# Performance work log

Hardware: AMD Instinct MI355X
Metric: run time of the kernel (lower is better)

The kernel has to match this reference:

```python
import jax, jax.numpy as jnp
import numpy as np

B, N = 16, 200000
R = 1_000_000
ITERS = 5
DAMPING = 0.5


def setup_inputs() -> dict:
    key = jax.random.key(0)
    ks = jax.random.split(key, 7)
    return {
        "evidence_logits": jax.random.normal(ks[0], (B, N), dtype=jnp.float32),
        "weights_t1": jax.random.uniform(ks[1], (R,), dtype=jnp.float32),
        "weights_t2": jax.random.uniform(ks[2], (R,), dtype=jnp.float32),
        "weights_t3": jax.random.uniform(ks[3], (R,), dtype=jnp.float32),
        "indices_t1": jax.random.randint(ks[4], (R, 2), 0, N, dtype=jnp.int64) if jax.config.jax_enable_x64 else jax.random.randint(ks[4], (R, 2), 0, N, dtype=jnp.int32),
        "indices_t2": jax.random.randint(ks[5], (R, 3), 0, N, dtype=jnp.int32),
        "indices_t3": jax.random.randint(ks[6], (R, 3), 0, N, dtype=jnp.int32),
    }


def _t1_messages(q, idx, w):
    # Template T1: p_a -> p_c
    a, c = idx[:, 0], idx[:, 1]
    q_a = q[:, a]            # (B, R)
    q_c = q[:, c]
    wb = w[None, :]
    delta = jnp.zeros_like(q)
    delta = delta.at[:, c].add(wb * q_a)
    delta = delta.at[:, a].add(wb * (q_c - 1.0))
    return delta


def _t2_messages(q, idx, w):
    # Template T2: p_a ^ p_b -> p_c
    a, b, c = idx[:, 0], idx[:, 1], idx[:, 2]
    q_a, q_b, q_c = q[:, a], q[:, b], q[:, c]
    wb = w[None, :]
    delta = jnp.zeros_like(q)
    delta = delta.at[:, c].add(wb * q_a * q_b)
    delta = delta.at[:, a].add(wb * q_b * (q_c - 1.0))
    delta = delta.at[:, b].add(wb * q_a * (q_c - 1.0))
    return delta


def _t3_messages(q, idx, w):
    # Template T3: p_a ^ !p_b -> p_c
    a, b, c = idx[:, 0], idx[:, 1], idx[:, 2]
    q_a, q_b, q_c = q[:, a], q[:, b], q[:, c]
    wb = w[None, :]
    delta = jnp.zeros_like(q)
    delta = delta.at[:, c].add(wb * q_a * (1.0 - q_b))
    delta = delta.at[:, a].add(wb * (1.0 - q_b) * (q_c - 1.0))
    delta = delta.at[:, b].add(wb * q_a * (1.0 - q_c))
    return delta


def reference(evidence_logits, weights_t1, weights_t2, weights_t3,
              indices_t1, indices_t2, indices_t3):
    curr_logits = evidence_logits
    curr_q = jax.nn.sigmoid(curr_logits)
    for _ in range(ITERS):
        total = (_t1_messages(curr_q, indices_t1, weights_t1)
                 + _t2_messages(curr_q, indices_t2, weights_t2)
                 + _t3_messages(curr_q, indices_t3, weights_t3))
        target_logits = evidence_logits + total
        curr_logits = (1.0 - DAMPING) * curr_logits + DAMPING * target_logits
        curr_q = jax.nn.sigmoid(curr_logits)
    return curr_q
```

## Files before the change

kernel.cpp:

```cpp
#include <hip/hip_runtime.h>

#define B 16
#define NN 200000
#define R 1000000
#define ITERS 5

__device__ __forceinline__ float sigmoidf_(float x) {
    return 1.0f / (1.0f + __expf(-x));
}

__global__ void cavi_init(const float* __restrict__ ev,
                          float* __restrict__ logits,
                          float* __restrict__ q_nb,
                          float* __restrict__ delta_nb) {
    int i = blockIdx.x * blockDim.x + threadIdx.x;
    if (i >= NN * B) return;
    int b = i & 15, n = i >> 4;
    float e = ev[b * NN + n];
    logits[b * NN + n] = e;
    q_nb[i] = sigmoidf_(e);
    delta_nb[i] = 0.0f;
}

__global__ void cavi_edges(const float* __restrict__ q,
                           float* __restrict__ delta,
                           const int* __restrict__ idx1, const float* __restrict__ w1,
                           const int* __restrict__ idx2, const float* __restrict__ w2,
                           const int* __restrict__ idx3, const float* __restrict__ w3) {
    int gid = blockIdx.x * blockDim.x + threadIdx.x;
    int b = gid & 15;
    int e = gid >> 4;
    if (e >= 3 * R) return;
    if (e < R) {
        int a = idx1[e * 2 + 0];
        int c = idx1[e * 2 + 1];
        float w = w1[e];
        float qa = q[a * B + b];
        float qc = q[c * B + b];
        atomicAdd(&delta[c * B + b], w * qa);
        atomicAdd(&delta[a * B + b], w * (qc - 1.0f));
    } else if (e < 2 * R) {
        int ei = e - R;
        int a  = idx2[ei * 3 + 0];
        int bb = idx2[ei * 3 + 1];
        int c  = idx2[ei * 3 + 2];
        float w = w2[ei];
        float qa = q[a * B + b];
        float qb = q[bb * B + b];
        float qc = q[c * B + b];
        atomicAdd(&delta[c * B + b],  w * qa * qb);
        atomicAdd(&delta[a * B + b],  w * qb * (qc - 1.0f));
        atomicAdd(&delta[bb * B + b], w * qa * (qc - 1.0f));
    } else {
        int ei = e - 2 * R;
        int a  = idx3[ei * 3 + 0];
        int bb = idx3[ei * 3 + 1];
        int c  = idx3[ei * 3 + 2];
        float w = w3[ei];
        float qa = q[a * B + b];
        float qb = q[bb * B + b];
        float qc = q[c * B + b];
        atomicAdd(&delta[c * B + b],  w * qa * (1.0f - qb));
        atomicAdd(&delta[a * B + b],  w * (1.0f - qb) * (qc - 1.0f));
        atomicAdd(&delta[bb * B + b], w * qa * (1.0f - qc));
    }
}

__global__ void cavi_update(const float* __restrict__ ev,
                            float* __restrict__ logits,
                            float* __restrict__ q_nb,
                            float* __restrict__ delta_nb,
                            int write_q) {
    int i = blockIdx.x * blockDim.x + threadIdx.x;
    if (i >= NN * B) return;
    int b = i & 15, n = i >> 4;
    float d = delta_nb[i];
    delta_nb[i] = 0.0f;
    float e  = ev[b * NN + n];
    float cl = logits[b * NN + n];
    float nl = 0.5f * cl + 0.5f * (e + d);
    float qv = sigmoidf_(nl);
    q_nb[i] = qv;
    logits[b * NN + n] = write_q ? qv : nl;
}

extern "C" void kernel_launch(void* const* d_in, const int* in_sizes, int n_in,
                              void* d_out, int out_size, void* d_ws, size_t ws_size,
                              hipStream_t stream) {
    const float* ev   = (const float*)d_in[0];
    const float* w1   = (const float*)d_in[1];
    const float* w2   = (const float*)d_in[2];
    const float* w3   = (const float*)d_in[3];
    const int*   idx1 = (const int*)d_in[4];
    const int*   idx2 = (const int*)d_in[5];
    const int*   idx3 = (const int*)d_in[6];

    float* logits   = (float*)d_out;
    float* q_nb     = (float*)d_ws;
    float* delta_nb = q_nb + (size_t)NN * B;

    const int ethreads = 256;
    const int nb_total = NN * B;
    const int nb_grid  = (nb_total + ethreads - 1) / ethreads;
    const int edge_total = 3 * R * B;
    const int edge_grid  = (edge_total + ethreads - 1) / ethreads;

    cavi_init<<<nb_grid, ethreads, 0, stream>>>(ev, logits, q_nb, delta_nb);
    for (int it = 0; it < ITERS; ++it) {
        cavi_edges<<<edge_grid, ethreads, 0, stream>>>(q_nb, delta_nb,
                                                       idx1, w1, idx2, w2, idx3, w3);
        cavi_update<<<nb_grid, ethreads, 0, stream>>>(ev, logits, q_nb, delta_nb,
                                                      it == ITERS - 1 ? 1 : 0);
    }
}
```

Baseline: 2.052 ms.

## Replace atomic scatter with CSR gather built per call for message passing

Builds a destination-indexed CSR (count, scan, fill) of all 8M edge contributions each call. Each iteration then becomes an atomic-free gather kernel that fuses the damping and sigmoid update, with q double-buffered. Evidence and output are transposed through LDS into node-major layout. This removes float atomics, but adds a per-call build pass with integer atomics and 96MB of extra workspace. It falls back to the old path if the workspace is too small.

```diff
diff --git a/kernel.cpp b/kernel.cpp
--- a/kernel.cpp
+++ b/kernel.cpp
@@ -4,15 +4,189 @@
 #define NN 200000
 #define R 1000000
 #define ITERS 5
+#define E_TOT (8 * R)
+#define SCAN_B 1024
+
+typedef unsigned int uint;
 
 __device__ __forceinline__ float sigmoidf_(float x) {
     return 1.0f / (1.0f + __expf(-x));
 }
 
-__global__ void cavi_init(const float* __restrict__ ev,
-                          float* __restrict__ logits,
-                          float* __restrict__ q_nb,
-                          float* __restrict__ delta_nb) {
+
+__global__ void cavi_zero_u32(uint* __restrict__ p, int n) {
+    int i = blockIdx.x * blockDim.x + threadIdx.x;
+    if (i < n) p[i] = 0u;
+}
+
+__global__ void cavi_count(const int* __restrict__ i1, const int* __restrict__ i2,
+                           const int* __restrict__ i3, uint* __restrict__ cnt) {
+    int e = blockIdx.x * blockDim.x + threadIdx.x;
+    if (e >= R) return;
+    int a1 = i1[2 * e], c1 = i1[2 * e + 1];
+    atomicAdd(&cnt[c1], 1u); atomicAdd(&cnt[a1], 1u);
+    int a2 = i2[3 * e], b2 = i2[3 * e + 1], c2 = i2[3 * e + 2];
+    atomicAdd(&cnt[c2], 1u); atomicAdd(&cnt[a2], 1u); atomicAdd(&cnt[b2], 1u);
+    int a3 = i3[3 * e], b3 = i3[3 * e + 1], c3 = i3[3 * e + 2];
+    atomicAdd(&cnt[c3], 1u); atomicAdd(&cnt[a3], 1u); atomicAdd(&cnt[b3], 1u);
+}
+
+__global__ void cavi_scan1(uint* __restrict__ cnt, uint* __restrict__ bsum) {
+    __shared__ uint s[SCAN_B];
+    int i = blockIdx.x * SCAN_B + threadIdx.x;
+    uint v = (i < NN) ? cnt[i] : 0u;
+    s[threadIdx.x] = v;
+    __syncthreads();
+    for (int d = 1; d < SCAN_B; d <<= 1) {
+        uint t = (threadIdx.x >= d) ? s[threadIdx.x - d] : 0u;
+        __syncthreads();
+        s[threadIdx.x] += t;
+        __syncthreads();
+    }
+    if (i < NN) cnt[i] = s[threadIdx.x] - v;
+    if (threadIdx.x == SCAN_B - 1) bsum[blockIdx.x] = s[threadIdx.x];
+}
+
+__global__ void cavi_scan2(uint* __restrict__ bsum, int nb) {
+    __shared__ uint s[256];
+    uint v = (threadIdx.x < (uint)nb) ? bsum[threadIdx.x] : 0u;
+    s[threadIdx.x] = v;
+    __syncthreads();
+    for (int d = 1; d < 256; d <<= 1) {
+        uint t = (threadIdx.x >= d) ? s[threadIdx.x - d] : 0u;
+        __syncthreads();
+        s[threadIdx.x] += t;
+        __syncthreads();
+    }
+    if (threadIdx.x < (uint)nb) bsum[threadIdx.x] = s[threadIdx.x] - v;
+    if (threadIdx.x == 255) bsum[nb] = s[255];
+}
+
+__global__ void cavi_scan3(const uint* __restrict__ cnt, const uint* __restrict__ bsum,
+                           uint* __restrict__ off, uint* __restrict__ cursor, int nb) {
+    int i = blockIdx.x * blockDim.x + threadIdx.x;
+    if (i < NN) {
+        uint v = cnt[i] + bsum[i >> 10];
+        off[i] = v;
+        cursor[i] = v;
+    } else if (i == NN) {
+        off[NN] = bsum[nb];
+    }
+}
+
+__device__ __forceinline__ void put_entry(int dest, int s1, uint md1, int s2, uint md2, float w,
+                                          uint* __restrict__ cursor, uint* __restrict__ m0,
+                                          uint* __restrict__ m1, float* __restrict__ wf) {
+    uint pos = atomicAdd(&cursor[dest], 1u);
+    m0[pos] = (uint)s1 | (md1 << 18);
+    m1[pos] = (uint)s2 | (md2 << 18);
+    wf[pos] = w;
+}
+
+__global__ void cavi_fill(const int* __restrict__ i1, const float* __restrict__ w1,
+                          const int* __restrict__ i2, const float* __restrict__ w2,
+                          const int* __restrict__ i3, const float* __restrict__ w3,
+                          uint* __restrict__ cursor, uint* __restrict__ m0,
+                          uint* __restrict__ m1, float* __restrict__ wf) {
+    int e = blockIdx.x * blockDim.x + threadIdx.x;
+    if (e >= R) return;
+    {
+        int a = i1[2 * e], c = i1[2 * e + 1];
+        float w = w1[e];
+        put_entry(c, a, 0u, 0, 3u, w, cursor, m0, m1, wf);
+        put_entry(a, c, 1u, 0, 3u, w, cursor, m0, m1, wf);
+    }
+    {
+        int a = i2[3 * e], b = i2[3 * e + 1], c = i2[3 * e + 2];
+        float w = w2[e];
+        put_entry(c, a, 0u, b, 0u, w, cursor, m0, m1, wf);
+        put_entry(a, b, 0u, c, 1u, w, cursor, m0, m1, wf);
+        put_entry(b, a, 0u, c, 1u, w, cursor, m0, m1, wf);
+    }
+    {
+        int a = i3[3 * e], b = i3[3 * e + 1], c = i3[3 * e + 2];
+        float w = w3[e];
+        put_entry(c, a, 0u, b, 2u, w, cursor, m0, m1, wf);
+        put_entry(a, b, 2u, c, 1u, w, cursor, m0, m1, wf);
+        put_entry(b, a, 0u, c, 2u, w, cursor, m0, m1, wf);
+    }
+}
+
+
+__global__ void cavi_init_tp(const float* __restrict__ ev, float* __restrict__ ev_nb,
+                             float* __restrict__ logits_nb, float* __restrict__ q0) {
+    __shared__ float lds[64 * 17];
+    int n0 = blockIdx.x * 64;
+    #pragma unroll
+    for (int p = 0; p < 4; ++p) {
+        int idx = p * 256 + threadIdx.x;
+        int b = idx >> 6, i = idx & 63;
+        lds[i * 17 + b] = ev[b * NN + n0 + i];
+    }
+    __syncthreads();
+    #pragma unroll
+    for (int p = 0; p < 4; ++p) {
+        int j = p * 256 + threadIdx.x;
+        int i = j >> 4, b = j & 15;
+        float v = lds[i * 17 + b];
+        int o = n0 * B + j;
+        ev_nb[o] = v;
+        logits_nb[o] = v;
+        q0[o] = sigmoidf_(v);
+    }
+}
+
+__global__ void cavi_out_tp(const float* __restrict__ q_nb, float* __restrict__ out) {
+    __shared__ float lds[64 * 17];
+    int n0 = blockIdx.x * 64;
+    #pragma unroll
+    for (int p = 0; p < 4; ++p) {
+        int j = p * 256 + threadIdx.x;
+        int i = j >> 4, b = j & 15;
+        lds[i * 17 + b] = q_nb[n0 * B + j];
+    }
+    __syncthreads();
+    #pragma unroll
+    for (int p = 0; p < 4; ++p) {
+        int idx = p * 256 + threadIdx.x;
+        int b = idx >> 6, i = idx & 63;
+        out[b * NN + n0 + i] = lds[i * 17 + b];
+    }
+}
+
+
+__global__ void cavi_main(const uint* __restrict__ off,
+                          const uint* __restrict__ m0, const uint* __restrict__ m1,
+                          const float* __restrict__ wf,
+                          const float* __restrict__ ev_nb, float* __restrict__ logits_nb,
+                          const float* __restrict__ q_in, float* __restrict__ q_out) {
+    int t = blockIdx.x * blockDim.x + threadIdx.x;
+    if (t >= NN * B) return;
+    int n = t >> 4, b = t & 15;
+    uint k0 = off[n], k1 = off[n + 1];
+    float acc = 0.0f;
+    for (uint k = k0; k < k1; ++k) {
+        uint a0 = m0[k], a1 = m1[k];
+        float w = wf[k];
+        float x = q_in[((a0 & 0x3FFFFu) << 4) + b];
+        uint md1 = a0 >> 18;
+        x = (md1 == 0u) ? x : ((md1 == 1u) ? x - 1.0f : 1.0f - x);
+        uint md2 = a1 >> 18;
+        float y = 1.0f;
+        if (md2 != 3u) {
+            float q2 = q_in[((a1 & 0x3FFFFu) << 4) + b];
+            y = (md2 == 0u) ? q2 : ((md2 == 1u) ? q2 - 1.0f : 1.0f - q2);
+        }
+        acc = fmaf(w * x, y, acc);
+    }
+    float nl = 0.5f * logits_nb[t] + 0.5f * (ev_nb[t] + acc);
+    logits_nb[t] = nl;
+    q_out[t] = sigmoidf_(nl);
+}
+
+
+__global__ void fb_init(const float* __restrict__ ev, float* __restrict__ logits,
+                        float* __restrict__ q_nb, float* __restrict__ delta_nb) {
     int i = blockIdx.x * blockDim.x + threadIdx.x;
     if (i >= NN * B) return;
     int b = i & 15, n = i >> 4;
@@ -22,61 +196,47 @@
     delta_nb[i] = 0.0f;
 }
 
-__global__ void cavi_edges(const float* __restrict__ q,
-                           float* __restrict__ delta,
-                           const int* __restrict__ idx1, const float* __restrict__ w1,
-                           const int* __restrict__ idx2, const float* __restrict__ w2,
-                           const int* __restrict__ idx3, const float* __restrict__ w3) {
+__global__ void fb_edges(const float* __restrict__ q, float* __restrict__ delta,
+                         const int* __restrict__ idx1, const float* __restrict__ w1,
+                         const int* __restrict__ idx2, const float* __restrict__ w2,
+                         const int* __restrict__ idx3, const float* __restrict__ w3) {
     int gid = blockIdx.x * blockDim.x + threadIdx.x;
     int b = gid & 15;
     int e = gid >> 4;
     if (e >= 3 * R) return;
     if (e < R) {
-        int a = idx1[e * 2 + 0];
-        int c = idx1[e * 2 + 1];
+        int a = idx1[e * 2 + 0], c = idx1[e * 2 + 1];
         float w = w1[e];
-        float qa = q[a * B + b];
-        float qc = q[c * B + b];
+        float qa = q[a * B + b], qc = q[c * B + b];
         atomicAdd(&delta[c * B + b], w * qa);
         atomicAdd(&delta[a * B + b], w * (qc - 1.0f));
     } else if (e < 2 * R) {
         int ei = e - R;
-        int a  = idx2[ei * 3 + 0];
-        int bb = idx2[ei * 3 + 1];
-        int c  = idx2[ei * 3 + 2];
+        int a = idx2[ei * 3], bb = idx2[ei * 3 + 1], c = idx2[ei * 3 + 2];
         float w = w2[ei];
-        float qa = q[a * B + b];
-        float qb = q[bb * B + b];
-        float qc = q[c * B + b];
-        atomicAdd(&delta[c * B + b],  w * qa * qb);
-        atomicAdd(&delta[a * B + b],  w * qb * (qc - 1.0f));
+        float qa = q[a * B + b], qb = q[bb * B + b], qc = q[c * B + b];
+        atomicAdd(&delta[c * B + b], w * qa * qb);
+        atomicAdd(&delta[a * B + b], w * qb * (qc - 1.0f));
         atomicAdd(&delta[bb * B + b], w * qa * (qc - 1.0f));
     } else {
         int ei = e - 2 * R;
-        int a  = idx3[ei * 3 + 0];
-        int bb = idx3[ei * 3 + 1];
-        int c  = idx3[ei * 3 + 2];
+        int a = idx3[ei * 3], bb = idx3[ei * 3 + 1], c = idx3[ei * 3 + 2];
         float w = w3[ei];
-        float qa = q[a * B + b];
-        float qb = q[bb * B + b];
-        float qc = q[c * B + b];
-        atomicAdd(&delta[c * B + b],  w * qa * (1.0f - qb));
-        atomicAdd(&delta[a * B + b],  w * (1.0f - qb) * (qc - 1.0f));
+        float qa = q[a * B + b], qb = q[bb * B + b], qc = q[c * B + b];
+        atomicAdd(&delta[c * B + b], w * qa * (1.0f - qb));
+        atomicAdd(&delta[a * B + b], w * (1.0f - qb) * (qc - 1.0f));
         atomicAdd(&delta[bb * B + b], w * qa * (1.0f - qc));
     }
 }
 
-__global__ void cavi_update(const float* __restrict__ ev,
-                            float* __restrict__ logits,
-                            float* __restrict__ q_nb,
-                            float* __restrict__ delta_nb,
-                            int write_q) {
+__global__ void fb_update(const float* __restrict__ ev, float* __restrict__ logits,
+                          float* __restrict__ q_nb, float* __restrict__ delta_nb, int write_q) {
     int i = blockIdx.x * blockDim.x + threadIdx.x;
     if (i >= NN * B) return;
     int b = i & 15, n = i >> 4;
     float d = delta_nb[i];
     delta_nb[i] = 0.0f;
-    float e  = ev[b * NN + n];
+    float e = ev[b * NN + n];
     float cl = logits[b * NN + n];
     float nl = 0.5f * cl + 0.5f * (e + d);
     float qv = sigmoidf_(nl);
@@ -84,32 +244,67 @@
     logits[b * NN + n] = write_q ? qv : nl;
 }
 
+
 extern "C" void kernel_launch(void* const* d_in, const int* in_sizes, int n_in,
                               void* d_out, int out_size, void* d_ws, size_t ws_size,
                               hipStream_t stream) {
-    const float* ev   = (const float*)d_in[0];
-    const float* w1   = (const float*)d_in[1];
-    const float* w2   = (const float*)d_in[2];
-    const float* w3   = (const float*)d_in[3];
-    const int*   idx1 = (const int*)d_in[4];
-    const int*   idx2 = (const int*)d_in[5];
-    const int*   idx3 = (const int*)d_in[6];
-
-    float* logits   = (float*)d_out;
-    float* q_nb     = (float*)d_ws;
-    float* delta_nb = q_nb + (size_t)NN * B;
-
-    const int ethreads = 256;
-    const int nb_total = NN * B;
-    const int nb_grid  = (nb_total + ethreads - 1) / ethreads;
-    const int edge_total = 3 * R * B;
-    const int edge_grid  = (edge_total + ethreads - 1) / ethreads;
-
-    cavi_init<<<nb_grid, ethreads, 0, stream>>>(ev, logits, q_nb, delta_nb);
+    const float* ev = (const float*)d_in[0];
+    const float* w1 = (const float*)d_in[1];
+    const float* w2 = (const float*)d_in[2];
+    const float* w3 = (const float*)d_in[3];
+    const int* i1 = (const int*)d_in[4];
+    const int* i2 = (const int*)d_in[5];
+    const int* i3 = (const int*)d_in[6];
+
+    const size_t NB = (size_t)NN * B;
+
+    float* ev_nb = (float*)d_ws;
+    float* logits_nb = ev_nb + NB;
+    float* q0 = logits_nb + NB;
+    float* q1 = q0 + NB;
+    uint* cnt = (uint*)(q1 + NB);
+    uint* off = cnt + NN;
+    uint* cursor = off + (NN + 1);
+    uint* bsum = cursor + NN;
+    uint* m0 = bsum + 272;
+    uint* m1 = m0 + (size_t)E_TOT;
+    float* wf = (float*)(m1 + (size_t)E_TOT);
+    size_t needed = (size_t)((char*)(wf + (size_t)E_TOT) - (char*)d_ws);
+
+    if (ws_size < needed) {
+        float* logits = (float*)d_out;
+        float* q_nb = (float*)d_ws;
+        float* delta_nb = q_nb + NB;
+        const int th = 256;
+        const int nbg = (int)((NB + th - 1) / th);
+        const int eg = (3 * R * B + th - 1) / th;
+        fb_init<<<nbg, th, 0, stream>>>(ev, logits, q_nb, delta_nb);
+        for (int it = 0; it < ITERS; ++it) {
+            fb_edges<<<eg, th, 0, stream>>>(q_nb, delta_nb, i1, w1, i2, w2, i3, w3);
+            fb_update<<<nbg, th, 0, stream>>>(ev, logits, q_nb, delta_nb, it == ITERS - 1 ? 1 : 0);
+        }
+        return;
+    }
+
+    const int th = 256;
+    const int scan_blocks = (NN + SCAN_B - 1) / SCAN_B;
+
+    cavi_zero_u32<<<(NN + th - 1) / th, th, 0, stream>>>(cnt, NN);
+    cavi_count<<<(R + th - 1) / th, th, 0, stream>>>(i1, i2, i3, cnt);
+    cavi_scan1<<<scan_blocks, SCAN_B, 0, stream>>>(cnt, bsum);
+    cavi_scan2<<<1, 256, 0, stream>>>(bsum, scan_blocks);
+    cavi_scan3<<<(NN + 1 + th) / th, th, 0, stream>>>(cnt, bsum, off, cursor, scan_blocks);
+    cavi_fill<<<(R + th - 1) / th, th, 0, stream>>>(i1, w1, i2, w2, i3, w3, cursor, m0, m1, wf);
+
+    cavi_init_tp<<<NN / 64, 256, 0, stream>>>(ev, ev_nb, logits_nb, q0);
+
+    const int mg = (int)(NB / th);
+    float* qi = q0;
+    float* qo = q1;
     for (int it = 0; it < ITERS; ++it) {
-        cavi_edges<<<edge_grid, ethreads, 0, stream>>>(q_nb, delta_nb,
-                                                       idx1, w1, idx2, w2, idx3, w3);
-        cavi_update<<<nb_grid, ethreads, 0, stream>>>(ev, logits, q_nb, delta_nb,
-                                                      it == ITERS - 1 ? 1 : 0);
-    }
-}
+        cavi_main<<<mg, th, 0, stream>>>(off, m0, m1, wf, ev_nb, logits_nb, qi, qo);
+        float* tmp = qi; qi = qo; qo = tmp;
+    }
+
+    cavi_out_tp<<<NN / 64, 256, 0, stream>>>(qi, (float*)d_out);
+}
```

Result: slower. 2.093 ms (+2.0%).
